# Performance work log

Measured on AMD Instinct MI355X. Metric: run time of the kernel, lower is better.

The kernel has to match this reference:

```python
import jax, jax.numpy as jnp
import numpy as np

ALPHA = 0.1
ONE_MINUS_ALPHA = 1.0 - ALPHA
EPSILON = 1e-3
B, T, F = 16, 4096, 512


def setup_inputs() -> dict:
    key = jax.random.key(0)
    x = jax.random.normal(key, (B, T, F), dtype=jnp.float32)
    # init_state: stack of running-mean zeros and running-mean-square ones
    state = jnp.stack([jnp.zeros((B, F), jnp.float32), jnp.ones((B, F), jnp.float32)], axis=0)  # [2,B,F]
    return {"x": x, "state": state}


def reference(x, state):
    # p = alpha * [x, x^2] stacked: [2, B, T, F]
    p = ALPHA * jnp.stack([x, x * x], axis=0)
    p_t = jnp.moveaxis(p, 2, 0)  # [T, 2, B, F] — scan over time

    def step(s, pt):
        s = pt + ONE_MINUS_ALPHA * s
        return s, s

    final_state, states = jax.lax.scan(step, state, p_t)  # states: [T, 2, B, F]
    state_vector = jnp.moveaxis(states, 0, 2)  # [2, B, T, F]
    mean_vector = state_vector[0]
    var_vector = state_vector[1] - mean_vector * mean_vector
    x_norm = (x - mean_vector) / jnp.sqrt(var_vector + EPSILON)
    return (x_norm, final_state)
```

## Files before the change

### kernel.cpp

```cpp
#include <hip/hip_runtime.h>


namespace {
constexpr int Bc = 16, Tc = 4096, Fc = 512;
constexpr int CL = 512;
constexpr int KH = 128;
constexpr int NCHUNK = Tc / CL;
constexpr float ALPHA = 0.1f;
constexpr float OMA = 0.9f;
constexpr float EPS = 1e-3f;
}

__global__ __launch_bounds__(256) void tn_kernel(const float* __restrict__ x,
                                                 const float* __restrict__ state,
                                                 float* __restrict__ out) {
    const int bid = blockIdx.x;
    const int fh = bid & 1;
    const int chunk = (bid >> 1) & (NCHUNK - 1);
    const int b = bid >> 4;
    const int f = fh * 256 + threadIdx.x;
    const int t0 = chunk * CL;

    const size_t base = ((size_t)b * Tc + t0) * Fc + f;
    const float* xp = x + base;

    float s_m, s_v;
    if (chunk == 0) {
        s_m = state[b * Fc + f];
        s_v = state[Bc * Fc + b * Fc + f];
    } else {
        s_m = 0.f;
        s_v = 0.f;
        const float* wp = xp - (size_t)KH * Fc;
#pragma unroll 16
        for (int i = 0; i < KH; ++i) {
            float xv = wp[(size_t)i * Fc];
            float px = ALPHA * xv;
            s_m = fmaf(OMA, s_m, px);
            s_v = fmaf(OMA, s_v, px * xv);
        }
    }

    float* op = out + base;
#pragma unroll 16
    for (int i = 0; i < CL; ++i) {
        float xv = xp[(size_t)i * Fc];
        float px = ALPHA * xv;
        s_m = fmaf(OMA, s_m, px);
        s_v = fmaf(OMA, s_v, px * xv);
        float var = fmaf(-s_m, s_m, s_v);
        float r = (xv - s_m) * rsqrtf(var + EPS);
        __builtin_nontemporal_store(r, &op[(size_t)i * Fc]);
    }

    if (chunk == NCHUNK - 1) {
        const size_t so = (size_t)Bc * Tc * Fc;
        out[so + (size_t)b * Fc + f] = s_m;
        out[so + (size_t)Bc * Fc + (size_t)b * Fc + f] = s_v;
    }
}

extern "C" void kernel_launch(void* const* d_in, const int* in_sizes, int n_in,
                              void* d_out, int out_size, void* d_ws, size_t ws_size,
                              hipStream_t stream) {
    const float* x = (const float*)d_in[0];
    const float* st = (const float*)d_in[1];
    float* out = (float*)d_out;

    dim3 grid(Bc * NCHUNK * 2);
    dim3 block(256);
    tn_kernel<<<grid, block, 0, stream>>>(x, st, out);
}
```

Before: 49.90 us.

## Replace halo warm-up with cooperative grid-sync exact carry propagation

```diff
diff --git a/kernel.cpp b/kernel.cpp
--- a/kernel.cpp
+++ b/kernel.cpp
@@ -1,19 +1,99 @@
 #include <hip/hip_runtime.h>
+#include <hip/hip_cooperative_groups.h>
 
+
+namespace cg = cooperative_groups;
 
 namespace {
 constexpr int Bc = 16, Tc = 4096, Fc = 512;
 constexpr int CL = 512;
 constexpr int KH = 128;
 constexpr int NCHUNK = Tc / CL;
+constexpr int LANES = 128;
 constexpr float ALPHA = 0.1f;
 constexpr float OMA = 0.9f;
 constexpr float EPS = 1e-3f;
 }
 
-__global__ __launch_bounds__(256) void tn_kernel(const float* __restrict__ x,
-                                                 const float* __restrict__ state,
-                                                 float* __restrict__ out) {
+__global__ __launch_bounds__(LANES, 2) void tn_coop(const float* __restrict__ x,
+                                                    const float* __restrict__ state,
+                                                    float* __restrict__ out,
+                                                    float* __restrict__ ws) {
+    __shared__ float stash[KH * LANES];
+
+    const int fq = blockIdx.x & 3;
+    const int chunk = (blockIdx.x >> 2) & (NCHUNK - 1);
+    const int b = blockIdx.x >> 5;
+    const int f = fq * LANES + threadIdx.x;
+    const int t0 = chunk * CL;
+
+    const size_t base = ((size_t)b * Tc + t0) * Fc + f;
+    const float* xp = x + base;
+    float* op = out + base;
+
+    float s_m, s_v;
+    if (chunk == 0) {
+        s_m = state[b * Fc + f];
+        s_v = state[Bc * Fc + b * Fc + f];
+    } else {
+        s_m = 0.f;
+        s_v = 0.f;
+    }
+
+#pragma unroll 16
+    for (int i = 0; i < KH; ++i) {
+        float xv = xp[(size_t)i * Fc];
+        stash[i * LANES + threadIdx.x] = xv;
+        float px = ALPHA * xv;
+        s_m = fmaf(OMA, s_m, px);
+        s_v = fmaf(OMA, s_v, px * xv);
+    }
+#pragma unroll 16
+    for (int i = KH; i < CL; ++i) {
+        float xv = xp[(size_t)i * Fc];
+        float px = ALPHA * xv;
+        s_m = fmaf(OMA, s_m, px);
+        s_v = fmaf(OMA, s_v, px * xv);
+        float var = fmaf(-s_m, s_m, s_v);
+        float r = (xv - s_m) * rsqrtf(var + EPS);
+        __builtin_nontemporal_store(r, &op[(size_t)i * Fc]);
+    }
+
+    const int widx = (b * NCHUNK + chunk) * Fc + f;
+    __hip_atomic_store(&ws[widx], s_m, __ATOMIC_RELAXED, __HIP_MEMORY_SCOPE_AGENT);
+    __hip_atomic_store(&ws[Bc * NCHUNK * Fc + widx], s_v, __ATOMIC_RELAXED, __HIP_MEMORY_SCOPE_AGENT);
+
+    if (chunk == NCHUNK - 1) {
+        const size_t so = (size_t)Bc * Tc * Fc;
+        out[so + (size_t)b * Fc + f] = s_m;
+        out[so + (size_t)Bc * Fc + (size_t)b * Fc + f] = s_v;
+    }
+
+    cg::this_grid().sync();
+
+    if (chunk == 0) {
+        s_m = state[b * Fc + f];
+        s_v = state[Bc * Fc + b * Fc + f];
+    } else {
+        const int pidx = (b * NCHUNK + chunk - 1) * Fc + f;
+        s_m = __hip_atomic_load(&ws[pidx], __ATOMIC_RELAXED, __HIP_MEMORY_SCOPE_AGENT);
+        s_v = __hip_atomic_load(&ws[Bc * NCHUNK * Fc + pidx], __ATOMIC_RELAXED, __HIP_MEMORY_SCOPE_AGENT);
+    }
+#pragma unroll 16
+    for (int i = 0; i < KH; ++i) {
+        float xv = stash[i * LANES + threadIdx.x];
+        float px = ALPHA * xv;
+        s_m = fmaf(OMA, s_m, px);
+        s_v = fmaf(OMA, s_v, px * xv);
+        float var = fmaf(-s_m, s_m, s_v);
+        float r = (xv - s_m) * rsqrtf(var + EPS);
+        __builtin_nontemporal_store(r, &op[(size_t)i * Fc]);
+    }
+}
+
+__global__ __launch_bounds__(256) void tn_halo(const float* __restrict__ x,
+                                               const float* __restrict__ state,
+                                               float* __restrict__ out) {
     const int bid = blockIdx.x;
     const int fh = bid & 1;
     const int chunk = (bid >> 1) & (NCHUNK - 1);
@@ -66,8 +146,14 @@
     const float* x = (const float*)d_in[0];
     const float* st = (const float*)d_in[1];
     float* out = (float*)d_out;
+    float* ws = (float*)d_ws;
 
-    dim3 grid(Bc * NCHUNK * 2);
-    dim3 block(256);
-    tn_kernel<<<grid, block, 0, stream>>>(x, st, out);
+    const size_t ws_needed = (size_t)2 * Bc * NCHUNK * Fc * sizeof(float);
+    if (ws_size >= ws_needed) {
+        void* args[] = {(void*)&x, (void*)&st, (void*)&out, (void*)&ws};
+        hipLaunchCooperativeKernel((const void*)tn_coop, dim3(Bc * NCHUNK * 4),
+                                   dim3(LANES), args, 0, stream);
+    } else {
+        tn_halo<<<dim3(Bc * NCHUNK * 2), dim3(256), 0, stream>>>(x, st, out);
+    }
 }
```

Result: slower. 130.7 us (+162.0%).
